# Optimization experiments

Measured on AMD Instinct MI355X. Metric: run time of the kernel, lower is better.

Reference implementation:

```python
import jax, jax.numpy as jnp
import numpy as np

TAU = 0.5
N, D = 8192, 128


def _l2norm(x):
    return x / jnp.linalg.norm(x, axis=-1, keepdims=True)


def setup_inputs() -> dict:
    key = jax.random.key(0)
    k1, k2 = jax.random.split(key)
    # Projected + L2-normalized node embeddings (output of GRACE._encode)
    z1 = _l2norm(jax.random.normal(k1, (N, D), dtype=jnp.float32))
    z2 = _l2norm(jax.random.normal(k2, (N, D), dtype=jnp.float32))
    return {"z1": z1, "z2": z2}


def reference(z1, z2):
    # refl_sim = exp(z1 z1^T / tau), between_sim = exp(z1 z2^T / tau)
    refl = jnp.exp(jnp.matmul(z1, z1.T) / TAU)        # [N, N]
    between = jnp.exp(jnp.matmul(z1, z2.T) / TAU)     # [N, N]

    def half_loss(a, b):
        # positives = diag(b); negatives = off-diag of a and b per row.
        # denom = (rowsum(a) - diag(a)) + (rowsum(b) - diag(b)) + diag(b)
        pos = jnp.diagonal(b)
        denom = a.sum(axis=1) - jnp.diagonal(a) + b.sum(axis=1)
        return -jnp.log(pos / denom)

    l1 = half_loss(refl, between)      # row view
    l2 = half_loss(refl.T, between.T)  # column view (diag is shared)
    ret = 0.5 * (l1 + l2)
    return ret.mean()
```

## Files before the change

### kernel.cpp

```cpp
#include <hip/hip_runtime.h>

typedef __attribute__((ext_vector_type(8))) short bf16x8;
typedef __attribute__((ext_vector_type(4))) float f32x4;
typedef unsigned short u16;

constexpr int N = 8192;
constexpr int D = 128;
constexpr float CEXP   = 2.8853900817779268f;
constexpr float BSCALE = 1.6986435688113073f;

#if __has_builtin(__builtin_amdgcn_exp2f)
__device__ __forceinline__ float fexp2(float x) { return __builtin_amdgcn_exp2f(x); }
#else
__device__ __forceinline__ float fexp2(float x) { return exp2f(x); }
#endif

__device__ __forceinline__ u16 f2bf(float x) {
  union { float f; unsigned u; } v;
  v.f = x;
  unsigned r = v.u + 0x7fffu + ((v.u >> 16) & 1u);
  return (u16)(r >> 16);
}

__global__ void convert_kernel(const float4* __restrict__ z1, const float4* __restrict__ z2,
                               uint2* __restrict__ o1, uint2* __restrict__ o2) {
  int t = blockIdx.x * 256 + threadIdx.x;
  float4 a = z1[t];
  float4 b = z2[t];
  uint2 pa, pb;
  pa.x = (unsigned)f2bf(a.x * BSCALE) | ((unsigned)f2bf(a.y * BSCALE) << 16);
  pa.y = (unsigned)f2bf(a.z * BSCALE) | ((unsigned)f2bf(a.w * BSCALE) << 16);
  pb.x = (unsigned)f2bf(b.x * BSCALE) | ((unsigned)f2bf(b.y * BSCALE) << 16);
  pb.y = (unsigned)f2bf(b.z * BSCALE) | ((unsigned)f2bf(b.w * BSCALE) << 16);
  o1[t] = pa;
  o2[t] = pb;
}

__global__ void zero_kernel(float* __restrict__ p, float* __restrict__ out) {
  int g = blockIdx.x * 256 + threadIdx.x;
  p[g] = 0.0f;
  if (g == 0) out[0] = 0.0f;
}

__device__ __forceinline__ void stage32k(char* lds, const char* gsrc, int soff, int doff) {
#pragma unroll
  for (int s = 0; s < 8; ++s) {
    __builtin_amdgcn_global_load_lds(
        (const __attribute__((address_space(1))) unsigned*)(gsrc + soff + s * 4096),
        (__attribute__((address_space(3))) unsigned*)(lds + doff + s * 4096), 16, 0, 0);
  }
}

__global__ __launch_bounds__(256, 2) void gemm_kernel(const u16* __restrict__ z1b,
                                                      const u16* __restrict__ z2b,
                                                      float* __restrict__ rowRefl,
                                                      float* __restrict__ rowBet,
                                                      float* __restrict__ colBet) {
  __shared__ __align__(16) char B0[32768];
  __shared__ __align__(16) char B1[32768];
  const int tid = threadIdx.x;
  const int l = tid & 63, w = tid >> 6;
  const int wr = w >> 1, wc = w & 1;
  const int lr = l & 15, lg = l >> 4;
  const int bi = blockIdx.x >> 3, jg = blockIdx.x & 7;
  const bool between = (jg & 4) != 0;
  const u16* bsrc = between ? z2b : z1b;
  const int j0 = (jg & 3) * 16;

  const int soff = (tid >> 4) * 256 + (((tid & 15) ^ (tid >> 4)) << 4);
  const int doff = tid * 16;

  stage32k(B0, (const char*)(z1b + (size_t)bi * 128 * D), soff, doff);
  __syncthreads();
  bf16x8 af[4][4];
#pragma unroll
  for (int m = 0; m < 4; ++m) {
    const int row = wr * 64 + m * 16 + lr;
#pragma unroll
    for (int kk = 0; kk < 4; ++kk)
      af[m][kk] = *(const bf16x8*)(B0 + row * 256 + (((kk * 4 + lg) ^ lr) << 4));
  }
  __syncthreads();

  stage32k(B0, (const char*)(bsrc + (size_t)j0 * 128 * D), soff, doff);

  float rowp[4][4];
#pragma unroll
  for (int m = 0; m < 4; ++m)
#pragma unroll
    for (int r = 0; r < 4; ++r) rowp[m][r] = 0.f;

  for (int t = 0; t < 16; ++t) {
    __syncthreads();
    const char* cur = (t & 1) ? B1 : B0;
    char* nxt = (t & 1) ? B0 : B1;
    if (t + 1 < 16)
      stage32k(nxt, (const char*)(bsrc + (size_t)(j0 + t + 1) * 128 * D), soff, doff);

    f32x4 acc[4][4];
    const f32x4 z4 = {0.f, 0.f, 0.f, 0.f};
    {
      bf16x8 bfr[4];
#pragma unroll
      for (int n = 0; n < 4; ++n) {
        const int row = wc * 64 + n * 16 + lr;
        bfr[n] = *(const bf16x8*)(cur + row * 256 + ((lg ^ lr) << 4));
      }
#pragma unroll
      for (int m = 0; m < 4; ++m)
#pragma unroll
        for (int n = 0; n < 4; ++n)
          acc[m][n] = __builtin_amdgcn_mfma_f32_16x16x32_bf16(af[m][0], bfr[n], z4, 0, 0, 0);
    }
#pragma unroll
    for (int kk = 1; kk < 4; ++kk) {
      bf16x8 bfr[4];
#pragma unroll
      for (int n = 0; n < 4; ++n) {
        const int row = wc * 64 + n * 16 + lr;
        bfr[n] = *(const bf16x8*)(cur + row * 256 + (((kk * 4 + lg) ^ lr) << 4));
      }
#pragma unroll
      for (int m = 0; m < 4; ++m)
#pragma unroll
        for (int n = 0; n < 4; ++n)
          acc[m][n] = __builtin_amdgcn_mfma_f32_16x16x32_bf16(af[m][kk], bfr[n], acc[m][n], 0, 0, 0);
    }

    if (!between) {
#pragma unroll
      for (int m = 0; m < 4; ++m)
#pragma unroll
        for (int n = 0; n < 4; ++n)
#pragma unroll
          for (int r = 0; r < 4; ++r) rowp[m][r] += fexp2(acc[m][n][r]);
    } else {
      float colp[4];
#pragma unroll
      for (int n = 0; n < 4; ++n) colp[n] = 0.f;
#pragma unroll
      for (int m = 0; m < 4; ++m)
#pragma unroll
        for (int n = 0; n < 4; ++n) {
          float v0 = fexp2(acc[m][n][0]), v1 = fexp2(acc[m][n][1]);
          float v2 = fexp2(acc[m][n][2]), v3 = fexp2(acc[m][n][3]);
          rowp[m][0] += v0;
          rowp[m][1] += v1;
          rowp[m][2] += v2;
          rowp[m][3] += v3;
          colp[n] += (v0 + v1) + (v2 + v3);
        }
#pragma unroll
      for (int n = 0; n < 4; ++n) {
        float c = colp[n];
        c += __shfl_xor(c, 16);
        c += __shfl_xor(c, 32);
        if (l < 16) atomicAdd(&colBet[(size_t)(j0 + t) * 128 + wc * 64 + n * 16 + l], c);
      }
    }
  }

  float* rowdst = between ? rowBet : rowRefl;
#pragma unroll
  for (int m = 0; m < 4; ++m)
#pragma unroll
    for (int r = 0; r < 4; ++r) {
      float s = rowp[m][r];
      s += __shfl_xor(s, 1);
      s += __shfl_xor(s, 2);
      s += __shfl_xor(s, 4);
      s += __shfl_xor(s, 8);
      if (lr == 0) atomicAdd(&rowdst[bi * 128 + wr * 64 + m * 16 + lg * 4 + r], s);
    }
}

__global__ void row_loss_kernel(const float* __restrict__ z1, const float* __restrict__ z2,
                                const float* __restrict__ rowRefl, const float* __restrict__ rowBet,
                                const float* __restrict__ colBet, float* __restrict__ rowLoss) {
  int gt = blockIdx.x * blockDim.x + threadIdx.x;
  int w = gt >> 6;
  int l = threadIdx.x & 63;
  if (w >= N) return;
  float a0 = z1[w * D + l], a1 = z1[w * D + 64 + l];
  float b0 = z2[w * D + l], b1 = z2[w * D + 64 + l];
  float d11 = a0 * a0 + a1 * a1;
  float d12 = a0 * b0 + a1 * b1;
#pragma unroll
  for (int mask = 1; mask < 64; mask <<= 1) {
    d11 += __shfl_xor(d11, mask);
    d12 += __shfl_xor(d12, mask);
  }
  if (l == 0) {
    float rdiag = fexp2(d11 * CEXP);
    float denom1 = rowRefl[w] - rdiag + rowBet[w];
    float denom2 = rowRefl[w] - rdiag + colBet[w];
    rowLoss[w] = 0.5f * (logf(denom1) + logf(denom2)) - 2.0f * d12;
  }
}

__global__ void final_reduce_kernel(const float* __restrict__ rowLoss, float* __restrict__ out) {
  int g = blockIdx.x * 256 + threadIdx.x;
  float s = rowLoss[g] * (1.0f / (float)N);
#pragma unroll
  for (int mask = 1; mask < 64; mask <<= 1) s += __shfl_xor(s, mask);
  if ((threadIdx.x & 63) == 0) atomicAdd(out, s);
}

extern "C" void kernel_launch(void* const* d_in, const int* in_sizes, int n_in,
                              void* d_out, int out_size, void* d_ws, size_t ws_size,
                              hipStream_t stream) {
  const float* z1 = (const float*)d_in[0];
  const float* z2 = (const float*)d_in[1];
  float* out = (float*)d_out;
  char* ws = (char*)d_ws;

  u16* z1b = (u16*)ws;
  u16* z2b = (u16*)(ws + (size_t)N * D * 2);
  float* rowRefl = (float*)(ws + (size_t)2 * N * D * 2);
  float* rowBet = rowRefl + N;
  float* colBet = rowBet + N;
  float* rowLoss = colBet + N;

  convert_kernel<<<(N * D / 4) / 256, 256, 0, stream>>>((const float4*)z1, (const float4*)z2,
                                                        (uint2*)z1b, (uint2*)z2b);
  zero_kernel<<<(3 * N) / 256, 256, 0, stream>>>(rowRefl, out);
  gemm_kernel<<<512, 256, 0, stream>>>(z1b, z2b, rowRefl, rowBet, colBet);
  row_loss_kernel<<<(N * 64) / 256, 256, 0, stream>>>(z1, z2, rowRefl, rowBet, colBet, rowLoss);
  final_reduce_kernel<<<32, 256, 0, stream>>>(rowLoss, out);
}
```

Measured before the change: 63.57 us.

## Halve GEMM column tile to 64 and raise occupancy to four blocks per CU

Result: slower. 77.01 us (+21.1%).

```diff
diff --git a/kernel.cpp b/kernel.cpp
--- a/kernel.cpp
+++ b/kernel.cpp
@@ -3,17 +3,12 @@
 typedef __attribute__((ext_vector_type(8))) short bf16x8;
 typedef __attribute__((ext_vector_type(4))) float f32x4;
 typedef unsigned short u16;
+typedef unsigned int u32;
 
 constexpr int N = 8192;
 constexpr int D = 128;
 constexpr float CEXP   = 2.8853900817779268f;
 constexpr float BSCALE = 1.6986435688113073f;
-
-#if __has_builtin(__builtin_amdgcn_exp2f)
-__device__ __forceinline__ float fexp2(float x) { return __builtin_amdgcn_exp2f(x); }
-#else
-__device__ __forceinline__ float fexp2(float x) { return exp2f(x); }
-#endif
 
 __device__ __forceinline__ u16 f2bf(float x) {
   union { float f; unsigned u; } v;
@@ -42,51 +37,54 @@
   if (g == 0) out[0] = 0.0f;
 }
 
-__device__ __forceinline__ void stage32k(char* lds, const char* gsrc, int soff, int doff) {
-#pragma unroll
-  for (int s = 0; s < 8; ++s) {
+__device__ __forceinline__ void stage16k(char* lds, const char* gsrc, int soff, int doff) {
+#pragma unroll
+  for (int s = 0; s < 4; ++s) {
     __builtin_amdgcn_global_load_lds(
-        (const __attribute__((address_space(1))) unsigned*)(gsrc + soff + s * 4096),
-        (__attribute__((address_space(3))) unsigned*)(lds + doff + s * 4096), 16, 0, 0);
-  }
-}
-
-__global__ __launch_bounds__(256, 2) void gemm_kernel(const u16* __restrict__ z1b,
+        (const __attribute__((address_space(1))) u32*)(gsrc + soff + s * 4096),
+        (__attribute__((address_space(3))) u32*)(lds + doff + s * 4096), 16, 0, 0);
+  }
+}
+
+__global__ __launch_bounds__(256, 4) void gemm_kernel(const u16* __restrict__ z1b,
                                                       const u16* __restrict__ z2b,
                                                       float* __restrict__ rowRefl,
                                                       float* __restrict__ rowBet,
                                                       float* __restrict__ colBet) {
-  __shared__ __align__(16) char B0[32768];
-  __shared__ __align__(16) char B1[32768];
+  __shared__ __align__(16) char B0[16384];
+  __shared__ __align__(16) char B1[16384];
   const int tid = threadIdx.x;
   const int l = tid & 63, w = tid >> 6;
-  const int wr = w >> 1, wc = w & 1;
   const int lr = l & 15, lg = l >> 4;
-  const int bi = blockIdx.x >> 3, jg = blockIdx.x & 7;
-  const bool between = (jg & 4) != 0;
+  const int bi = blockIdx.x >> 4;
+  const int jg = blockIdx.x & 15;
+  const bool between = jg >= 8;
   const u16* bsrc = between ? z2b : z1b;
-  const int j0 = (jg & 3) * 16;
+  const int j0 = (jg & 7) * 16;
 
   const int soff = (tid >> 4) * 256 + (((tid & 15) ^ (tid >> 4)) << 4);
   const int doff = tid * 16;
 
-  stage32k(B0, (const char*)(z1b + (size_t)bi * 128 * D), soff, doff);
+  stage16k(B0, (const char*)(z1b + (size_t)bi * 128 * D), soff, doff);
+  stage16k(B1, (const char*)(z1b + (size_t)(bi * 128 + 64) * D), soff, doff);
   __syncthreads();
-  bf16x8 af[4][4];
-#pragma unroll
-  for (int m = 0; m < 4; ++m) {
-    const int row = wr * 64 + m * 16 + lr;
-#pragma unroll
-    for (int kk = 0; kk < 4; ++kk)
-      af[m][kk] = *(const bf16x8*)(B0 + row * 256 + (((kk * 4 + lg) ^ lr) << 4));
+  bf16x8 af[2][4];
+  {
+    const char* Asrc = (w & 2) ? B1 : B0;
+    const int rbase = (w & 1) * 32 + lr;
+#pragma unroll
+    for (int m = 0; m < 2; ++m)
+#pragma unroll
+      for (int kk = 0; kk < 4; ++kk)
+        af[m][kk] = *(const bf16x8*)(Asrc + (rbase + m * 16) * 256 + (((kk * 4 + lg) ^ lr) << 4));
   }
   __syncthreads();
 
-  stage32k(B0, (const char*)(bsrc + (size_t)j0 * 128 * D), soff, doff);
-
-  float rowp[4][4];
-#pragma unroll
-  for (int m = 0; m < 4; ++m)
+  stage16k(B0, (const char*)(bsrc + (size_t)j0 * 64 * D), soff, doff);
+
+  float rowp[2][4];
+#pragma unroll
+  for (int m = 0; m < 2; ++m)
 #pragma unroll
     for (int r = 0; r < 4; ++r) rowp[m][r] = 0.f;
 
@@ -95,19 +93,17 @@
     const char* cur = (t & 1) ? B1 : B0;
     char* nxt = (t & 1) ? B0 : B1;
     if (t + 1 < 16)
-      stage32k(nxt, (const char*)(bsrc + (size_t)(j0 + t + 1) * 128 * D), soff, doff);
-
-    f32x4 acc[4][4];
+      stage16k(nxt, (const char*)(bsrc + (size_t)(j0 + t + 1) * 64 * D), soff, doff);
+
+    f32x4 acc[2][4];
     const f32x4 z4 = {0.f, 0.f, 0.f, 0.f};
     {
       bf16x8 bfr[4];
 #pragma unroll
-      for (int n = 0; n < 4; ++n) {
-        const int row = wc * 64 + n * 16 + lr;
-        bfr[n] = *(const bf16x8*)(cur + row * 256 + ((lg ^ lr) << 4));
-      }
-#pragma unroll
-      for (int m = 0; m < 4; ++m)
+      for (int n = 0; n < 4; ++n)
+        bfr[n] = *(const bf16x8*)(cur + (n * 16 + lr) * 256 + ((lg ^ lr) << 4));
+#pragma unroll
+      for (int m = 0; m < 2; ++m)
 #pragma unroll
         for (int n = 0; n < 4; ++n)
           acc[m][n] = __builtin_amdgcn_mfma_f32_16x16x32_bf16(af[m][0], bfr[n], z4, 0, 0, 0);
@@ -116,12 +112,10 @@
     for (int kk = 1; kk < 4; ++kk) {
       bf16x8 bfr[4];
 #pragma unroll
-      for (int n = 0; n < 4; ++n) {
-        const int row = wc * 64 + n * 16 + lr;
-        bfr[n] = *(const bf16x8*)(cur + row * 256 + (((kk * 4 + lg) ^ lr) << 4));
-      }
-#pragma unroll
-      for (int m = 0; m < 4; ++m)
+      for (int n = 0; n < 4; ++n)
+        bfr[n] = *(const bf16x8*)(cur + (n * 16 + lr) * 256 + (((kk * 4 + lg) ^ lr) << 4));
+#pragma unroll
+      for (int m = 0; m < 2; ++m)
 #pragma unroll
         for (int n = 0; n < 4; ++n)
           acc[m][n] = __builtin_amdgcn_mfma_f32_16x16x32_bf16(af[m][kk], bfr[n], acc[m][n], 0, 0, 0);
@@ -129,21 +123,21 @@
 
     if (!between) {
 #pragma unroll
-      for (int m = 0; m < 4; ++m)
+      for (int m = 0; m < 2; ++m)
 #pragma unroll
         for (int n = 0; n < 4; ++n)
 #pragma unroll
-          for (int r = 0; r < 4; ++r) rowp[m][r] += fexp2(acc[m][n][r]);
+          for (int r = 0; r < 4; ++r) rowp[m][r] += exp2f(acc[m][n][r]);
     } else {
       float colp[4];
 #pragma unroll
       for (int n = 0; n < 4; ++n) colp[n] = 0.f;
 #pragma unroll
-      for (int m = 0; m < 4; ++m)
+      for (int m = 0; m < 2; ++m)
 #pragma unroll
         for (int n = 0; n < 4; ++n) {
-          float v0 = fexp2(acc[m][n][0]), v1 = fexp2(acc[m][n][1]);
-          float v2 = fexp2(acc[m][n][2]), v3 = fexp2(acc[m][n][3]);
+          float v0 = exp2f(acc[m][n][0]), v1 = exp2f(acc[m][n][1]);
+          float v2 = exp2f(acc[m][n][2]), v3 = exp2f(acc[m][n][3]);
           rowp[m][0] += v0;
           rowp[m][1] += v1;
           rowp[m][2] += v2;
@@ -155,14 +149,14 @@
         float c = colp[n];
         c += __shfl_xor(c, 16);
         c += __shfl_xor(c, 32);
-        if (l < 16) atomicAdd(&colBet[(size_t)(j0 + t) * 128 + wc * 64 + n * 16 + l], c);
+        if (l < 16) atomicAdd(&colBet[(j0 + t) * 64 + n * 16 + l], c);
       }
     }
   }
 
   float* rowdst = between ? rowBet : rowRefl;
 #pragma unroll
-  for (int m = 0; m < 4; ++m)
+  for (int m = 0; m < 2; ++m)
 #pragma unroll
     for (int r = 0; r < 4; ++r) {
       float s = rowp[m][r];
@@ -170,7 +164,7 @@
       s += __shfl_xor(s, 2);
       s += __shfl_xor(s, 4);
       s += __shfl_xor(s, 8);
-      if (lr == 0) atomicAdd(&rowdst[bi * 128 + wr * 64 + m * 16 + lg * 4 + r], s);
+      if (lr == 0) atomicAdd(&rowdst[bi * 128 + w * 32 + m * 16 + lg * 4 + r], s);
     }
 }
 
@@ -191,7 +185,7 @@
     d12 += __shfl_xor(d12, mask);
   }
   if (l == 0) {
-    float rdiag = fexp2(d11 * CEXP);
+    float rdiag = exp2f(d11 * CEXP);
     float denom1 = rowRefl[w] - rdiag + rowBet[w];
     float denom2 = rowRefl[w] - rdiag + colBet[w];
     rowLoss[w] = 0.5f * (logf(denom1) + logf(denom2)) - 2.0f * d12;
@@ -224,7 +218,7 @@
   convert_kernel<<<(N * D / 4) / 256, 256, 0, stream>>>((const float4*)z1, (const float4*)z2,
                                                         (uint2*)z1b, (uint2*)z2b);
   zero_kernel<<<(3 * N) / 256, 256, 0, stream>>>(rowRefl, out);
-  gemm_kernel<<<512, 256, 0, stream>>>(z1b, z2b, rowRefl, rowBet, colBet);
+  gemm_kernel<<<1024, 256, 0, stream>>>(z1b, z2b, rowRefl, rowBet, colBet);
   row_loss_kernel<<<(N * 64) / 256, 256, 0, stream>>>(z1, z2, rowRefl, rowBet, colBet, rowLoss);
   final_reduce_kernel<<<32, 256, 0, stream>>>(rowLoss, out);
 }
```
